# Kernel optimization log

Hardware: AMD Instinct MI355X
Metric: run time of the kernel (lower is better)

The kernel has to match this reference:

```python
import jax, jax.numpy as jnp
import numpy as np

B, T, I, H = 32, 512, 512, 1024


def setup_inputs() -> dict:
    key = jax.random.key(0)
    ks = jax.random.split(key, 9)
    k = 1.0 / np.sqrt(H)  # torch nn.RNN init: U(-1/sqrt(H), 1/sqrt(H))
    u = lambda kk, sh: jax.random.uniform(kk, sh, jnp.float32, -k, k)
    return {
        "x": jax.random.normal(ks[0], (B, T, I), jnp.float32),
        "W_ih0": u(ks[1], (H, I)),
        "W_hh0": u(ks[2], (H, H)),
        "b_ih0": u(ks[3], (H,)),
        "b_hh0": u(ks[4], (H,)),
        "W_ih1": u(ks[5], (H, H)),
        "W_hh1": u(ks[6], (H, H)),
        "b_ih1": u(ks[7], (H,)),
        "b_hh1": u(ks[8], (H,)),
    }


def _rnn_layer(x_tbi, Wih, Whh, bih, bhh):
    # Precompute input projection for all timesteps: [T, B, H]
    xw = jnp.einsum('tbi,hi->tbh', x_tbi, Wih) + bih + bhh
    h0 = jnp.zeros((x_tbi.shape[1], Whh.shape[0]), x_tbi.dtype)

    def step(h, xw_t):
        h = jnp.tanh(xw_t + h @ Whh.T)
        return h, h

    _, hs = jax.lax.scan(step, h0, xw)
    return hs  # [T, B, H]


def reference(x, W_ih0, W_hh0, b_ih0, b_hh0, W_ih1, W_hh1, b_ih1, b_hh1):
    x_tbi = jnp.transpose(x, (1, 0, 2))  # [T, B, I]
    h1 = _rnn_layer(x_tbi, W_ih0, W_hh0, b_ih0, b_hh0)
    h2 = _rnn_layer(h1, W_ih1, W_hh1, b_ih1, b_hh1)
    return jnp.transpose(h2, (1, 0, 2))  # [B, T, H]
```

## Files before the change

kernel.cpp:

```cpp
#include <hip/hip_runtime.h>
#include <hip/hip_bf16.h>


#define B_ 32
#define T_ 512
#define I_ 512
#define H_ 1024

typedef __attribute__((ext_vector_type(8))) short short8;
typedef __attribute__((ext_vector_type(4))) float float4v;

#define OFF_XBF   0ull
#define OFF_H1    16777216ull
#define OFF_HPING 50397184ull
#define OFF_FLAGS 50528256ull

#define WAIT_VM0() asm volatile("s_waitcnt vmcnt(0)" ::: "memory")
#define CFENCE()   asm volatile("" ::: "memory")

#define LDF(f, base, O) \
  asm volatile("global_load_dwordx4 %0, %1, off offset:%2 sc1" \
               : "=v"(f) : "v"(base), "n"(O) : "memory")

#define LD8(F, S, BASE, OB) \
  LDF(F[S+0], BASE, OB+0);   LDF(F[S+1], BASE, OB+64); \
  LDF(F[S+2], BASE, OB+128); LDF(F[S+3], BASE, OB+192); \
  LDF(F[S+4], BASE, OB+256); LDF(F[S+5], BASE, OB+320); \
  LDF(F[S+6], BASE, OB+384); LDF(F[S+7], BASE, OB+448)

#define VMW8(N, F, S) \
  asm volatile("s_waitcnt vmcnt(" #N ")" \
               : "+v"(F[S+0]), "+v"(F[S+1]), "+v"(F[S+2]), "+v"(F[S+3]), \
                 "+v"(F[S+4]), "+v"(F[S+5]), "+v"(F[S+6]), "+v"(F[S+7]))

#define MFMA_B(acc, f, kb) \
  acc = __builtin_amdgcn_mfma_f32_16x16x32_bf16( \
      f, *reinterpret_cast<const short8*>(ldsW + (kb) * 512 + lofs), acc, 0, 0, 0)

#define MF8(F, S, KB) \
  MFMA_B(accA, F[S+0], KB+0); MFMA_B(accB, F[S+1], KB+1); \
  MFMA_B(accA, F[S+2], KB+2); MFMA_B(accB, F[S+3], KB+3); \
  MFMA_B(accA, F[S+4], KB+4); MFMA_B(accB, F[S+5], KB+5); \
  MFMA_B(accA, F[S+6], KB+6); MFMA_B(accB, F[S+7], KB+7)

__device__ __forceinline__ float fast_tanh(float x) {
  float z = fminf(2.885390081777927f * x, 60.0f);
  float e = __builtin_amdgcn_exp2f(z);
  return 1.0f - 2.0f * __builtin_amdgcn_rcpf(e + 1.0f);
}

__device__ __forceinline__ void wait_layer(unsigned* fbase, int lane, int wid, unsigned s) {
  unsigned* p = fbase + (((unsigned)lane << 1) + wid) * 16;
  while (__hip_atomic_load(p, __ATOMIC_RELAXED, __HIP_MEMORY_SCOPE_AGENT) < s)
    __builtin_amdgcn_s_sleep(1);
  CFENCE();
}

__global__ __launch_bounds__(128)
void rnn_fused(const float* __restrict__ Wih0, const float* __restrict__ Whh0,
               const float* __restrict__ bih0, const float* __restrict__ bhh0,
               const float* __restrict__ Wih1, const float* __restrict__ Whh1,
               const float* __restrict__ bih1, const float* __restrict__ bhh1,
               const __hip_bfloat16* __restrict__ x_bf,
               __hip_bfloat16* __restrict__ h1buf,
               __hip_bfloat16* __restrict__ hping,
               float* __restrict__ out,
               unsigned* __restrict__ flags)
{
  __shared__ unsigned short ldsW[16 * 2048];
  const int tid  = threadIdx.x;
  const int wgid = blockIdx.x;
  const bool isL1 = (wgid >= 64);
  const int wg   = isL1 ? wgid - 64 : wgid;
  const int KIN  = isL1 ? H_ : I_;
  const int KTOT = KIN + H_;
  const float* Wih = isL1 ? Wih1 : Wih0;
  const float* Whh = isL1 ? Whh1 : Whh0;

  for (int idx = tid; idx < 16 * KTOT; idx += 128) {
    int c = idx / KTOT;
    int k = idx - c * KTOT;
    float w = (k < KIN) ? Wih[(size_t)(wg * 16 + c) * KIN + k]
                        : Whh[(size_t)(wg * 16 + c) * H_ + (k - KIN)];
    __hip_bfloat16 hb = __float2bfloat16(w);
    int pos = ((k >> 5) * 64 + ((k >> 3) & 3) * 16 + c) * 8 + (k & 7);
    ldsW[pos] = *reinterpret_cast<unsigned short*>(&hb);
  }

  const int lane  = tid & 63;
  const int wid   = tid >> 6;
  const int col   = wg * 16 + (lane & 15);
  const float biasv = isL1 ? (bih1[col] + bhh1[col]) : (bih0[col] + bhh0[col]);
  const int arow  = wid * 16 + (lane & 15);
  const int ksub  = ((lane >> 4) & 3) * 8;
  const int lofs  = lane * 8;
  const int rbase = wid * 16 + (lane >> 4) * 4;
  const int r0    = (lane & 1) ? 2 : 0;
  const int colp  = col & ~1;

  unsigned* fl0 = flags;
  unsigned* fl1 = flags + 128 * 16;
  unsigned* myflag = (isL1 ? fl1 : fl0) + (((unsigned)wg << 1) + wid) * 16;

  __syncthreads();

  if (!isL1) {
    for (int s = 0; s < T_; ++s) {
      float4v accA = {biasv, biasv, biasv, biasv};
      float4v accB = {0.f, 0.f, 0.f, 0.f};
      const __hip_bfloat16* a0 = x_bf + (size_t)arow * (T_ * I_) + (size_t)s * I_ + ksub;
#pragma unroll
      for (int kb = 0; kb < 16; ++kb) {
        short8 av = *reinterpret_cast<const short8*>(a0 + kb * 32);
        MFMA_B(accA, av, kb);
      }
      if (s > 0) wait_layer(fl0, lane, wid, (unsigned)s);
      const __hip_bfloat16* a1 = h1buf + (size_t)s * (B_ * H_) + (size_t)arow * H_ + ksub;
      short8 g[32];
      LD8(g, 0, a1, 0);  LD8(g, 8, a1, 512);  LD8(g, 16, a1, 1024);  LD8(g, 24, a1, 1536);
      VMW8(24, g, 0);   MF8(g, 0, 16);
      VMW8(16, g, 8);   MF8(g, 8, 24);
      VMW8(8,  g, 16);  MF8(g, 16, 32);
      VMW8(0,  g, 24);  MF8(g, 24, 40);

      __hip_bfloat16* hd = h1buf + (size_t)(s + 1) * (B_ * H_);
      float hv[4];
#pragma unroll
      for (int r = 0; r < 4; ++r) hv[r] = fast_tanh(accA[r] + accB[r]);
#pragma unroll
      for (int r = 0; r < 4; ++r) {
        float other = __shfl_xor(hv[r], 1, 64);
        float lo = (lane & 1) ? other : hv[r];
        float hi = (lane & 1) ? hv[r] : other;
        if (r == r0 || r == r0 + 1) {
          __hip_bfloat16 l16 = __float2bfloat16(lo), h16 = __float2bfloat16(hi);
          unsigned pk = (unsigned)*(unsigned short*)&l16 | ((unsigned)*(unsigned short*)&h16 << 16);
          unsigned* dst = (unsigned*)(hd + (size_t)(rbase + r) * H_ + colp);
          __hip_atomic_store(dst, pk, __ATOMIC_RELAXED, __HIP_MEMORY_SCOPE_AGENT);
        }
      }
      WAIT_VM0();
      if (lane == 0)
        __hip_atomic_store(myflag, (unsigned)(s + 1), __ATOMIC_RELAXED, __HIP_MEMORY_SCOPE_AGENT);
    }
  } else {
    for (int t = 0; t < T_; ++t) {
      float4v accA = {biasv, biasv, biasv, biasv};
      float4v accB = {0.f, 0.f, 0.f, 0.f};
      wait_layer(fl0, lane, wid, (unsigned)(t + 1));
      if (t > 0) wait_layer(fl1, lane, wid, (unsigned)t);
      const __hip_bfloat16* aA = h1buf + (size_t)(t + 1) * (B_ * H_) + (size_t)arow * H_ + ksub;
      const __hip_bfloat16* aB = hping + (size_t)(t & 1) * (B_ * H_) + (size_t)arow * H_ + ksub;
      short8 g[32], h[32];
      LD8(g, 0, aA, 0);  LD8(g, 8, aA, 512);  LD8(g, 16, aA, 1024);  LD8(g, 24, aA, 1536);
      VMW8(24, g, 0);   MF8(g, 0, 0);    LD8(h, 0, aB, 0);
      VMW8(24, g, 8);   MF8(g, 8, 8);    LD8(h, 8, aB, 512);
      VMW8(24, g, 16);  MF8(g, 16, 16);  LD8(h, 16, aB, 1024);
      VMW8(24, g, 24);  MF8(g, 24, 24);  LD8(h, 24, aB, 1536);
      VMW8(24, h, 0);   MF8(h, 0, 32);
      VMW8(16, h, 8);   MF8(h, 8, 40);
      VMW8(8,  h, 16);  MF8(h, 16, 48);
      VMW8(0,  h, 24);  MF8(h, 24, 56);

      __hip_bfloat16* hd = hping + (size_t)((t + 1) & 1) * (B_ * H_);
      float hv[4];
#pragma unroll
      for (int r = 0; r < 4; ++r) hv[r] = fast_tanh(accA[r] + accB[r]);
      float lov[4], hiv[4];
#pragma unroll
      for (int r = 0; r < 4; ++r) {
        float other = __shfl_xor(hv[r], 1, 64);
        lov[r] = (lane & 1) ? other : hv[r];
        hiv[r] = (lane & 1) ? hv[r] : other;
        if (r == r0 || r == r0 + 1) {
          __hip_bfloat16 l16 = __float2bfloat16(lov[r]), h16 = __float2bfloat16(hiv[r]);
          unsigned pk = (unsigned)*(unsigned short*)&l16 | ((unsigned)*(unsigned short*)&h16 << 16);
          unsigned* dst = (unsigned*)(hd + (size_t)(rbase + r) * H_ + colp);
          __hip_atomic_store(dst, pk, __ATOMIC_RELAXED, __HIP_MEMORY_SCOPE_AGENT);
        }
      }
      WAIT_VM0();
      if (lane == 0)
        __hip_atomic_store(myflag, (unsigned)(t + 1), __ATOMIC_RELAXED, __HIP_MEMORY_SCOPE_AGENT);
#pragma unroll
      for (int r = 0; r < 4; ++r) {
        if (r == r0 || r == r0 + 1) {
          float2 f2; f2.x = lov[r]; f2.y = hiv[r];
          *(float2*)(out + (size_t)(rbase + r) * (T_ * H_) + (size_t)t * H_ + colp) = f2;
        }
      }
    }
  }
}

__global__ void prep_kernel(const float* __restrict__ x, unsigned long long* __restrict__ x64,
                            unsigned* __restrict__ h1z, unsigned* __restrict__ hpz,
                            unsigned* __restrict__ flags)
{
  int i = blockIdx.x * 256 + threadIdx.x;
  if (i < (B_ * T_ * I_) / 4) {
    const float4* x4 = (const float4*)x;
    float4 v = x4[i];
    __hip_bfloat16 b0 = __float2bfloat16(v.x), b1 = __float2bfloat16(v.y);
    __hip_bfloat16 b2 = __float2bfloat16(v.z), b3 = __float2bfloat16(v.w);
    unsigned long long r = (unsigned long long)*(unsigned short*)&b0
                         | ((unsigned long long)*(unsigned short*)&b1 << 16)
                         | ((unsigned long long)*(unsigned short*)&b2 << 32)
                         | ((unsigned long long)*(unsigned short*)&b3 << 48);
    x64[i] = r;
  }
  if (i < 16384) __hip_atomic_store(h1z + i, 0u, __ATOMIC_RELAXED, __HIP_MEMORY_SCOPE_AGENT);
  if (i < 32768) __hip_atomic_store(hpz + i, 0u, __ATOMIC_RELAXED, __HIP_MEMORY_SCOPE_AGENT);
  if (i < 4096)  __hip_atomic_store(flags + i, 0u, __ATOMIC_RELAXED, __HIP_MEMORY_SCOPE_AGENT);
}

extern "C" void kernel_launch(void* const* d_in, const int* in_sizes, int n_in,
                              void* d_out, int out_size, void* d_ws, size_t ws_size,
                              hipStream_t stream)
{
  const float* x    = (const float*)d_in[0];
  const float* Wih0 = (const float*)d_in[1];
  const float* Whh0 = (const float*)d_in[2];
  const float* bih0 = (const float*)d_in[3];
  const float* bhh0 = (const float*)d_in[4];
  const float* Wih1 = (const float*)d_in[5];
  const float* Whh1 = (const float*)d_in[6];
  const float* bih1 = (const float*)d_in[7];
  const float* bhh1 = (const float*)d_in[8];
  float* out = (float*)d_out;
  char* ws = (char*)d_ws;

  __hip_bfloat16* x_bf  = (__hip_bfloat16*)(ws + OFF_XBF);
  __hip_bfloat16* h1buf = (__hip_bfloat16*)(ws + OFF_H1);
  __hip_bfloat16* hping = (__hip_bfloat16*)(ws + OFF_HPING);
  unsigned* flags = (unsigned*)(ws + OFF_FLAGS);

  prep_kernel<<<(B_ * T_ * I_ / 4 + 255) / 256, 256, 0, stream>>>(
      x, (unsigned long long*)x_bf, (unsigned*)h1buf, (unsigned*)hping, flags);

  rnn_fused<<<128, 128, 0, stream>>>(Wih0, Whh0, bih0, bhh0,
                                     Wih1, Whh1, bih1, bhh1,
                                     x_bf, h1buf, hping, out, flags);
}
```

Before: 2.829 ms.

## Replace flag-based step synchronization with poisoned-data polling on hidden-state buffers

Drops the per-step flag counters, the vmcnt(0) drain and the flag store that carried the dependency between timesteps. Instead the hidden-state buffers are pre-filled with a NaN-like poison pattern, and consumers reload the loaded fragments until none of them hold the poison bits. Layer 2 gets a full-history h2 buffer when the workspace is large enough, with the old ping-pong and flag path kept as a fallback. The aim is to remove the extra round-trip of the flag handshake, at the cost of a much larger prep fill (about 33 MB per buffer), repeated reloads while polling, and reliance on the poison check holding for real bf16 tanh outputs.

```diff
diff --git a/kernel.cpp b/kernel.cpp
--- a/kernel.cpp
+++ b/kernel.cpp
@@ -12,8 +12,11 @@
 
 #define OFF_XBF   0ull
 #define OFF_H1    16777216ull
-#define OFF_HPING 50397184ull
+#define OFF_H2    50397184ull
 #define OFF_FLAGS 50528256ull
+#define NEED_FULL 84017152ull
+
+#define POIS 0x7F807F80u
 
 #define WAIT_VM0() asm volatile("s_waitcnt vmcnt(0)" ::: "memory")
 #define CFENCE()   asm volatile("" ::: "memory")
@@ -33,6 +36,25 @@
                : "+v"(F[S+0]), "+v"(F[S+1]), "+v"(F[S+2]), "+v"(F[S+3]), \
                  "+v"(F[S+4]), "+v"(F[S+5]), "+v"(F[S+6]), "+v"(F[S+7]))
 
+__device__ __forceinline__ bool any8_stale(const short8* F, int S) {
+  union { short8 s; unsigned u[4]; } x;
+  unsigned o = 0u;
+#pragma unroll
+  for (int i = 0; i < 8; ++i) { x.s = F[S+i]; o |= x.u[0] | x.u[1] | x.u[2] | x.u[3]; }
+  return (o & 0x40004000u) != 0u;
+}
+
+#define POLL8(F, S, BASE, OB) \
+  do { \
+    while (__any((int)any8_stale(F, S))) { \
+      __builtin_amdgcn_s_sleep(1); \
+      LD8(F, S, BASE, OB); \
+      asm volatile("s_waitcnt vmcnt(0)" \
+                   : "+v"(F[S+0]), "+v"(F[S+1]), "+v"(F[S+2]), "+v"(F[S+3]), \
+                     "+v"(F[S+4]), "+v"(F[S+5]), "+v"(F[S+6]), "+v"(F[S+7])); \
+    } \
+  } while (0)
+
 #define MFMA_B(acc, f, kb) \
   acc = __builtin_amdgcn_mfma_f32_16x16x32_bf16( \
       f, *reinterpret_cast<const short8*>(ldsW + (kb) * 512 + lofs), acc, 0, 0, 0)
@@ -49,13 +71,14 @@
   return 1.0f - 2.0f * __builtin_amdgcn_rcpf(e + 1.0f);
 }
 
-__device__ __forceinline__ void wait_layer(unsigned* fbase, int lane, int wid, unsigned s) {
+__device__ __forceinline__ void wait_flags(unsigned* fbase, int lane, int wid, unsigned s) {
   unsigned* p = fbase + (((unsigned)lane << 1) + wid) * 16;
   while (__hip_atomic_load(p, __ATOMIC_RELAXED, __HIP_MEMORY_SCOPE_AGENT) < s)
     __builtin_amdgcn_s_sleep(1);
   CFENCE();
 }
 
+template<bool FULL>
 __global__ __launch_bounds__(128)
 void rnn_fused(const float* __restrict__ Wih0, const float* __restrict__ Whh0,
                const float* __restrict__ bih0, const float* __restrict__ bhh0,
@@ -63,7 +86,7 @@
                const float* __restrict__ bih1, const float* __restrict__ bhh1,
                const __hip_bfloat16* __restrict__ x_bf,
                __hip_bfloat16* __restrict__ h1buf,
-               __hip_bfloat16* __restrict__ hping,
+               __hip_bfloat16* __restrict__ h2buf,
                float* __restrict__ out,
                unsigned* __restrict__ flags)
 {
@@ -98,9 +121,7 @@
   const int r0    = (lane & 1) ? 2 : 0;
   const int colp  = col & ~1;
 
-  unsigned* fl0 = flags;
-  unsigned* fl1 = flags + 128 * 16;
-  unsigned* myflag = (isL1 ? fl1 : fl0) + (((unsigned)wg << 1) + wid) * 16;
+  unsigned* myflag = flags + (((unsigned)wg << 1) + wid) * 16;
 
   __syncthreads();
 
@@ -114,14 +135,13 @@
         short8 av = *reinterpret_cast<const short8*>(a0 + kb * 32);
         MFMA_B(accA, av, kb);
       }
-      if (s > 0) wait_layer(fl0, lane, wid, (unsigned)s);
       const __hip_bfloat16* a1 = h1buf + (size_t)s * (B_ * H_) + (size_t)arow * H_ + ksub;
       short8 g[32];
       LD8(g, 0, a1, 0);  LD8(g, 8, a1, 512);  LD8(g, 16, a1, 1024);  LD8(g, 24, a1, 1536);
-      VMW8(24, g, 0);   MF8(g, 0, 16);
-      VMW8(16, g, 8);   MF8(g, 8, 24);
-      VMW8(8,  g, 16);  MF8(g, 16, 32);
-      VMW8(0,  g, 24);  MF8(g, 24, 40);
+      VMW8(24, g, 0);   POLL8(g, 0, a1, 0);     MF8(g, 0, 16);
+      VMW8(16, g, 8);   POLL8(g, 8, a1, 512);   MF8(g, 8, 24);
+      VMW8(8,  g, 16);  POLL8(g, 16, a1, 1024); MF8(g, 16, 32);
+      VMW8(0,  g, 24);  POLL8(g, 24, a1, 1536); MF8(g, 24, 40);
 
       __hip_bfloat16* hd = h1buf + (size_t)(s + 1) * (B_ * H_);
       float hv[4];
@@ -139,30 +159,32 @@
           __hip_atomic_store(dst, pk, __ATOMIC_RELAXED, __HIP_MEMORY_SCOPE_AGENT);
         }
       }
-      WAIT_VM0();
-      if (lane == 0)
-        __hip_atomic_store(myflag, (unsigned)(s + 1), __ATOMIC_RELAXED, __HIP_MEMORY_SCOPE_AGENT);
     }
   } else {
     for (int t = 0; t < T_; ++t) {
       float4v accA = {biasv, biasv, biasv, biasv};
       float4v accB = {0.f, 0.f, 0.f, 0.f};
-      wait_layer(fl0, lane, wid, (unsigned)(t + 1));
-      if (t > 0) wait_layer(fl1, lane, wid, (unsigned)t);
       const __hip_bfloat16* aA = h1buf + (size_t)(t + 1) * (B_ * H_) + (size_t)arow * H_ + ksub;
-      const __hip_bfloat16* aB = hping + (size_t)(t & 1) * (B_ * H_) + (size_t)arow * H_ + ksub;
+      const __hip_bfloat16* aB;
+      if constexpr (FULL) {
+        aB = h2buf + (size_t)t * (B_ * H_) + (size_t)arow * H_ + ksub;
+      } else {
+        if (t > 0) wait_flags(flags, lane, wid, (unsigned)t);
+        aB = h2buf + (size_t)(t & 1) * (B_ * H_) + (size_t)arow * H_ + ksub;
+      }
       short8 g[32], h[32];
       LD8(g, 0, aA, 0);  LD8(g, 8, aA, 512);  LD8(g, 16, aA, 1024);  LD8(g, 24, aA, 1536);
-      VMW8(24, g, 0);   MF8(g, 0, 0);    LD8(h, 0, aB, 0);
-      VMW8(24, g, 8);   MF8(g, 8, 8);    LD8(h, 8, aB, 512);
-      VMW8(24, g, 16);  MF8(g, 16, 16);  LD8(h, 16, aB, 1024);
-      VMW8(24, g, 24);  MF8(g, 24, 24);  LD8(h, 24, aB, 1536);
-      VMW8(24, h, 0);   MF8(h, 0, 32);
-      VMW8(16, h, 8);   MF8(h, 8, 40);
-      VMW8(8,  h, 16);  MF8(h, 16, 48);
-      VMW8(0,  h, 24);  MF8(h, 24, 56);
-
-      __hip_bfloat16* hd = hping + (size_t)((t + 1) & 1) * (B_ * H_);
+      VMW8(24, g, 0);   POLL8(g, 0, aA, 0);     MF8(g, 0, 0);    LD8(h, 0, aB, 0);
+      VMW8(24, g, 8);   POLL8(g, 8, aA, 512);   MF8(g, 8, 8);    LD8(h, 8, aB, 512);
+      VMW8(24, g, 16);  POLL8(g, 16, aA, 1024); MF8(g, 16, 16);  LD8(h, 16, aB, 1024);
+      VMW8(24, g, 24);  POLL8(g, 24, aA, 1536); MF8(g, 24, 24);  LD8(h, 24, aB, 1536);
+      VMW8(24, h, 0);   if constexpr (FULL) POLL8(h, 0, aB, 0);     MF8(h, 0, 32);
+      VMW8(16, h, 8);   if constexpr (FULL) POLL8(h, 8, aB, 512);   MF8(h, 8, 40);
+      VMW8(8,  h, 16);  if constexpr (FULL) POLL8(h, 16, aB, 1024); MF8(h, 16, 48);
+      VMW8(0,  h, 24);  if constexpr (FULL) POLL8(h, 24, aB, 1536); MF8(h, 24, 56);
+
+      __hip_bfloat16* hd = FULL ? h2buf + (size_t)(t + 1) * (B_ * H_)
+                                : h2buf + (size_t)((t + 1) & 1) * (B_ * H_);
       float hv[4];
 #pragma unroll
       for (int r = 0; r < 4; ++r) hv[r] = fast_tanh(accA[r] + accB[r]);
@@ -179,9 +201,11 @@
           __hip_atomic_store(dst, pk, __ATOMIC_RELAXED, __HIP_MEMORY_SCOPE_AGENT);
         }
       }
-      WAIT_VM0();
-      if (lane == 0)
-        __hip_atomic_store(myflag, (unsigned)(t + 1), __ATOMIC_RELAXED, __HIP_MEMORY_SCOPE_AGENT);
+      if constexpr (!FULL) {
+        WAIT_VM0();
+        if (lane == 0)
+          __hip_atomic_store(myflag, (unsigned)(t + 1), __ATOMIC_RELAXED, __HIP_MEMORY_SCOPE_AGENT);
+      }
 #pragma unroll
       for (int r = 0; r < 4; ++r) {
         if (r == r0 || r == r0 + 1) {
@@ -194,11 +218,11 @@
 }
 
 __global__ void prep_kernel(const float* __restrict__ x, unsigned long long* __restrict__ x64,
-                            unsigned* __restrict__ h1z, unsigned* __restrict__ hpz,
-                            unsigned* __restrict__ flags)
+                            unsigned* __restrict__ h1, unsigned* __restrict__ h2,
+                            unsigned* __restrict__ flags, int full)
 {
-  int i = blockIdx.x * 256 + threadIdx.x;
-  if (i < (B_ * T_ * I_) / 4) {
+  unsigned i = blockIdx.x * 256 + threadIdx.x;
+  if (i < 2097152u) {
     const float4* x4 = (const float4*)x;
     float4 v = x4[i];
     __hip_bfloat16 b0 = __float2bfloat16(v.x), b1 = __float2bfloat16(v.y);
@@ -209,9 +233,17 @@
                          | ((unsigned long long)*(unsigned short*)&b3 << 48);
     x64[i] = r;
   }
-  if (i < 16384) __hip_atomic_store(h1z + i, 0u, __ATOMIC_RELAXED, __HIP_MEMORY_SCOPE_AGENT);
-  if (i < 32768) __hip_atomic_store(hpz + i, 0u, __ATOMIC_RELAXED, __HIP_MEMORY_SCOPE_AGENT);
-  if (i < 4096)  __hip_atomic_store(flags + i, 0u, __ATOMIC_RELAXED, __HIP_MEMORY_SCOPE_AGENT);
+  const unsigned NH = 513u * 16384u;
+  if (i < NH) {
+    unsigned v = (i < 16384u) ? 0u : POIS;
+    __hip_atomic_store(h1 + i, v, __ATOMIC_RELAXED, __HIP_MEMORY_SCOPE_AGENT);
+    if (full)
+      __hip_atomic_store(h2 + i, v, __ATOMIC_RELAXED, __HIP_MEMORY_SCOPE_AGENT);
+  }
+  if (!full) {
+    if (i < 32768u) __hip_atomic_store(h2 + i, 0u, __ATOMIC_RELAXED, __HIP_MEMORY_SCOPE_AGENT);
+    if (i < 2048u)  __hip_atomic_store(flags + i, 0u, __ATOMIC_RELAXED, __HIP_MEMORY_SCOPE_AGENT);
+  }
 }
 
 extern "C" void kernel_launch(void* const* d_in, const int* in_sizes, int n_in,
@@ -232,13 +264,21 @@
 
   __hip_bfloat16* x_bf  = (__hip_bfloat16*)(ws + OFF_XBF);
   __hip_bfloat16* h1buf = (__hip_bfloat16*)(ws + OFF_H1);
-  __hip_bfloat16* hping = (__hip_bfloat16*)(ws + OFF_HPING);
+  __hip_bfloat16* h2buf = (__hip_bfloat16*)(ws + OFF_H2);
   unsigned* flags = (unsigned*)(ws + OFF_FLAGS);
 
-  prep_kernel<<<(B_ * T_ * I_ / 4 + 255) / 256, 256, 0, stream>>>(
-      x, (unsigned long long*)x_bf, (unsigned*)h1buf, (unsigned*)hping, flags);
-
-  rnn_fused<<<128, 128, 0, stream>>>(Wih0, Whh0, bih0, bhh0,
-                                     Wih1, Whh1, bih1, bhh1,
-                                     x_bf, h1buf, hping, out, flags);
-}
+  const bool full = (ws_size >= NEED_FULL);
+
+  prep_kernel<<<32832, 256, 0, stream>>>(x, (unsigned long long*)x_bf,
+                                         (unsigned*)h1buf, (unsigned*)h2buf,
+                                         flags, full ? 1 : 0);
+
+  if (full)
+    rnn_fused<true><<<128, 128, 0, stream>>>(Wih0, Whh0, bih0, bhh0,
+                                             Wih1, Whh1, bih1, bhh1,
+                                             x_bf, h1buf, h2buf, out, flags);
+  else
+    rnn_fused<false><<<128, 128, 0, stream>>>(Wih0, Whh0, bih0, bhh0,
+                                              Wih1, Whh1, bih1, bhh1,
+                                              x_bf, h1buf, h2buf, out, flags);
+}
```

Result: slower. 3.235 ms (+14.4%).
